# Kernel tuning notes

Measured on AMD Instinct MI355X. Metric: run time of the kernel, lower is better.

## Reference

```python
import jax, jax.numpy as jnp
import numpy as np
import math

H, HK, D = 16, 4, 128  # n_heads, n_kv_heads, head_dim
WINDOW = 1024
ROPE_BASE = 10000.0
EPS = 1e-6

def _rope_cos_sin(T, dtype):
    inv_freq = 1.0 / (ROPE_BASE ** (jnp.arange(0, D, 2, dtype=jnp.float32) / D))
    ang = jnp.arange(T, dtype=jnp.float32)[:, None] * inv_freq[None, :]  # [T, D/2]
    cos = jnp.concatenate([jnp.cos(ang), jnp.cos(ang)], axis=-1)  # [T, D]
    sin = jnp.concatenate([jnp.sin(ang), jnp.sin(ang)], axis=-1)
    return cos.astype(dtype), sin.astype(dtype)

def _rotate_half(x):
    x1, x2 = jnp.split(x, 2, axis=-1)
    return jnp.concatenate([-x2, x1], axis=-1)

def _apply_rope(t, cos, sin):
    # t: [B, h, T, D]; cos/sin: [T, D]
    return t * cos[None, None] + _rotate_half(t) * sin[None, None]

def setup_inputs() -> dict:
    key = jax.random.key(0)
    ks = jax.random.split(key, 7)
    d = H * D
    s = 1.0 / math.sqrt(d)
    return {
        "x": jax.random.normal(ks[0], (2, 2048, d), jnp.float32),
        "wq": jax.random.normal(ks[1], (H * D, d), jnp.float32) * s,
        "wk": jax.random.normal(ks[2], (HK * D, d), jnp.float32) * s,
        "wv": jax.random.normal(ks[3], (HK * D, d), jnp.float32) * s,
        "wo": jax.random.normal(ks[4], (d, H * D), jnp.float32) * s,
        "gamma_q": jnp.ones((D,), jnp.float32),
        "gamma_k": jnp.ones((D,), jnp.float32),
    }

def reference(x, wq, wk, wv, wo, gamma_q, gamma_k):
    B, T, d = x.shape
    G = H // HK  # query heads per kv head
    # projections (Linear stores [out, in]) -> [B, h, T, D]
    q = jnp.einsum('btd,ed->bte', x, wq).reshape(B, T, H, D).transpose(0, 2, 1, 3)
    k = jnp.einsum('btd,ed->bte', x, wk).reshape(B, T, HK, D).transpose(0, 2, 1, 3)
    v = jnp.einsum('btd,ed->bte', x, wv).reshape(B, T, HK, D).transpose(0, 2, 1, 3)
    cos, sin = _rope_cos_sin(T, x.dtype)
    q = _apply_rope(q, cos, sin)
    k = _apply_rope(k, cos, sin)
    # QK-norm: L2 normalize then learned per-dim scale
    q = q / (jnp.linalg.norm(q, axis=-1, keepdims=True) + EPS) * gamma_q
    k = k / (jnp.linalg.norm(k, axis=-1, keepdims=True) + EPS) * gamma_k
    # GQA: group query heads instead of materializing repeated K/V
    qg = q.reshape(B, HK, G, T, D)
    att = jnp.einsum('bkgtd,bksd->bkgts', qg, k) / math.sqrt(D)  # [B,HK,G,T,T]
    i = jnp.arange(T)
    diff = i[:, None] - i[None, :]
    bad = (diff < 0) | (diff > WINDOW)  # causal OR beyond sliding window
    att = jnp.where(bad[None, None, None], -jnp.inf, att)
    p = jax.nn.softmax(att, axis=-1)
    y = jnp.einsum('bkgts,bksd->bkgtd', p, v)  # [B,HK,G,T,D]
    y = y.reshape(B, H, T, D).transpose(0, 2, 1, 3).reshape(B, T, H * D)
    y = jnp.einsum('bte,de->btd', y, wo)
    return y
```

## Files before the change

kernel.cpp:

```cpp
#include <hip/hip_runtime.h>
#include <cstdint>
#include <cstddef>

typedef unsigned short u16;
typedef short bf16x8 __attribute__((ext_vector_type(8)));
typedef float f32x4 __attribute__((ext_vector_type(4)));

#define MFMA(a,b,c) __builtin_amdgcn_mfma_f32_16x16x32_bf16(a,b,c,0,0,0)

__device__ __forceinline__ u16 f2bf(float f) {
  unsigned u = __builtin_bit_cast(unsigned, f);
  u += 0x7fffu + ((u >> 16) & 1u);
  return (u16)(u >> 16);
}
__device__ __forceinline__ float bf2f(u16 b) {
  return __builtin_bit_cast(float, (unsigned)b << 16);
}
__device__ __forceinline__ float exp2_hw(float x) {
  float r;
  asm("v_exp_f32 %0, %1" : "=v"(r) : "v"(x));
  return r;
}
__device__ __forceinline__ void gl_lds16(const void* g, void* l) {
  __builtin_amdgcn_global_load_lds(
      (const __attribute__((address_space(1))) void*)g,
      (__attribute__((address_space(3))) void*)l, 16, 0, 0);
}
template <int N>
__device__ __forceinline__ void wait_vmcnt() {
  if constexpr (N == 0) asm volatile("s_waitcnt vmcnt(0)" ::: "memory");
  else if constexpr (N == 3) asm volatile("s_waitcnt vmcnt(3)" ::: "memory");
  else if constexpr (N == 4) asm volatile("s_waitcnt vmcnt(4)" ::: "memory");
}

__global__ __launch_bounds__(256) void cvt_all(const float* __restrict__ x,
                                               const float* __restrict__ wq,
                                               const float* __restrict__ wk,
                                               const float* __restrict__ wv,
                                               const float* __restrict__ wo,
                                               u16* __restrict__ xb,
                                               u16* __restrict__ wqkvb,
                                               u16* __restrict__ wob) {
  int idx = (blockIdx.x * 256 + threadIdx.x) * 4;
  const float* src;
  u16* dst;
  if (idx < 8388608) { src = x + idx; dst = xb + idx; }
  else if (idx < 12582912) { src = wq + (idx - 8388608); dst = wqkvb + (idx - 8388608); }
  else if (idx < 13631488) { src = wk + (idx - 12582912); dst = wqkvb + (idx - 8388608); }
  else if (idx < 14680064) { src = wv + (idx - 13631488); dst = wqkvb + (idx - 8388608); }
  else if (idx < 18874368) { src = wo + (idx - 14680064); dst = wob + (idx - 14680064); }
  else return;
  float4 v = *(const float4*)src;
  ushort4 o = {f2bf(v.x), f2bf(v.y), f2bf(v.z), f2bf(v.w)};
  *(ushort4*)dst = o;
}

__global__ __launch_bounds__(256) void rope_table(float* __restrict__ ctab,
                                                  float* __restrict__ stab) {
  int i = blockIdx.x * 256 + threadIdx.x;
  int t = i >> 6, f = i & 63;
  float inv_freq = powf(10000.0f, -(2.0f * f) / 128.0f);
  float ang = (float)t * inv_freq;
  ctab[i] = cosf(ang);
  stab[i] = sinf(ang);
}

template <int BM, int BN, int OUT_F32>
__global__ __launch_bounds__(512, 2) void gemm_nt8(const u16* __restrict__ A,
                                                   const u16* __restrict__ Bw,
                                                   void* __restrict__ Cout,
                                                   int M, int N, int K) {
  constexpr int PHASES = (BM * BN == 65536) ? 2 : 1;
  constexpr int WN = BN / 64;
  constexpr int WM = 8 / WN;
  constexpr int M_SUB = BM / WM;
  constexpr int M_REP = M_SUB / 16;
  constexpr int MRP = M_REP / PHASES;
  constexpr int ACH = BM / 128;
  constexpr int BCH = BN / 128;
  constexpr int LPT = ACH + BCH;

  __shared__ u16 As[3][BM * 32];
  __shared__ u16 Bs[3][BN * 32];

  const int tid = threadIdx.x;
  const int lane = tid & 63;
  const int wv = tid >> 6;
  const int l16 = lane & 15, lhi = lane >> 4;
  const int wm = wv / WN, wn = wv % WN;
  const int m0 = blockIdx.y * BM;
  const int n0 = blockIdx.x * BN;
  const int nt = K >> 5;

  const int srow = lane >> 2;
  const int scolb = ((lane & 3) * 16) ^ ((((lane >> 3) & 3)) << 4);

  auto stageA = [&](int buf, int kt, int ch) {
    const char* src = (const char*)A +
        ((size_t)(m0 + ch * 16 + srow) * K + (size_t)kt * 32) * 2 + scolb;
    gl_lds16(src, (char*)As[buf] + ch * 1024);
  };
  auto stageB = [&](int buf, int kt, int ch) {
    const char* src = (const char*)Bw +
        ((size_t)(n0 + ch * 16 + srow) * K + (size_t)kt * 32) * 2 + scolb;
    gl_lds16(src, (char*)Bs[buf] + ch * 1024);
  };
  auto readA = [&](const u16* Ab, int mi) -> bf16x8 {
    int row = wm * M_SUB + mi * 16 + l16;
    return *(const bf16x8*)((const char*)Ab + row * 64 +
                            ((lhi * 16) ^ (((row >> 1) & 3) << 4)));
  };
  auto readB = [&](const u16* Bb, int ni) -> bf16x8 {
    int row = wn * 64 + ni * 16 + l16;
    return *(const bf16x8*)((const char*)Bb + row * 64 +
                            ((lhi * 16) ^ (((row >> 1) & 3) << 4)));
  };

  f32x4 acc[M_REP][4] = {};

#pragma unroll
  for (int i = 0; i < ACH; ++i) stageA(0, 0, wv + 8 * i);
#pragma unroll
  for (int i = 0; i < BCH; ++i) stageB(0, 0, wv + 8 * i);
#pragma unroll
  for (int i = 0; i < ACH; ++i) stageA(1, 1, wv + 8 * i);
#pragma unroll
  for (int i = 0; i < BCH; ++i) stageB(1, 1, wv + 8 * i);
  wait_vmcnt<LPT>();
  __builtin_amdgcn_sched_barrier(0);
  __builtin_amdgcn_s_barrier();
  __builtin_amdgcn_sched_barrier(0);

  int p = 0;
  for (int t = 0; t < nt; ++t) {
    const u16* Ab = As[p];
    const u16* Bb = Bs[p];
    int pb = p + 2; if (pb >= 3) pb -= 3;
    const bool do_stage = (t + 2 < nt);

    bf16x8 bfrag[4], afrag[MRP];
#pragma unroll
    for (int ni = 0; ni < 4; ++ni) bfrag[ni] = readB(Bb, ni);
#pragma unroll
    for (int mi = 0; mi < MRP; ++mi) afrag[mi] = readA(Ab, mi);
    if (do_stage) {
#pragma unroll
      for (int i = 0; i < ACH; i += PHASES) stageA(pb, t + 2, wv + 8 * i);
#pragma unroll
      for (int i = 0; i < BCH; i += PHASES) stageB(pb, t + 2, wv + 8 * i);
    }
    if (PHASES == 1) { if (do_stage) wait_vmcnt<LPT>(); else wait_vmcnt<0>(); }
    __builtin_amdgcn_sched_barrier(0);
    __builtin_amdgcn_s_barrier();
    __builtin_amdgcn_sched_barrier(0);
    __builtin_amdgcn_s_setprio(1);
#pragma unroll
    for (int mi = 0; mi < MRP; ++mi)
#pragma unroll
      for (int ni = 0; ni < 4; ++ni)
        acc[mi][ni] = MFMA(afrag[mi], bfrag[ni], acc[mi][ni]);
    __builtin_amdgcn_s_setprio(0);
    __builtin_amdgcn_sched_barrier(0);
    __builtin_amdgcn_s_barrier();
    __builtin_amdgcn_sched_barrier(0);

    if (PHASES == 2) {
#pragma unroll
      for (int mi = 0; mi < MRP; ++mi) afrag[mi] = readA(Ab, MRP + mi);
      if (do_stage) {
#pragma unroll
        for (int i = 1; i < ACH; i += PHASES) stageA(pb, t + 2, wv + 8 * i);
#pragma unroll
        for (int i = 1; i < BCH; i += PHASES) stageB(pb, t + 2, wv + 8 * i);
      }
      if (do_stage) wait_vmcnt<LPT>(); else wait_vmcnt<0>();
      __builtin_amdgcn_sched_barrier(0);
      __builtin_amdgcn_s_barrier();
      __builtin_amdgcn_sched_barrier(0);
      __builtin_amdgcn_s_setprio(1);
#pragma unroll
      for (int mi = 0; mi < MRP; ++mi)
#pragma unroll
        for (int ni = 0; ni < 4; ++ni)
          acc[MRP + mi][ni] = MFMA(afrag[mi], bfrag[ni], acc[MRP + mi][ni]);
      __builtin_amdgcn_s_setprio(0);
      __builtin_amdgcn_sched_barrier(0);
      __builtin_amdgcn_s_barrier();
      __builtin_amdgcn_sched_barrier(0);
    }
    p = (p + 1 == 3) ? 0 : p + 1;
  }

#pragma unroll
  for (int mi = 0; mi < M_REP; ++mi)
#pragma unroll
    for (int ni = 0; ni < 4; ++ni) {
      int col = n0 + wn * 64 + ni * 16 + l16;
#pragma unroll
      for (int j = 0; j < 4; ++j) {
        int row = m0 + wm * M_SUB + mi * 16 + lhi * 4 + j;
        float v = acc[mi][ni][j];
        if (OUT_F32)
          ((float*)Cout)[(size_t)row * N + col] = v;
        else
          ((u16*)Cout)[(size_t)row * N + col] = f2bf(v);
      }
    }
}

template <int NH>
__global__ __launch_bounds__(256) void rope_norm(const u16* __restrict__ raw,
                                                 u16* __restrict__ out,
                                                 const float* __restrict__ ctab,
                                                 const float* __restrict__ stab,
                                                 const float* __restrict__ gamma,
                                                 int stride, int coloff, float scale) {
  int gw = blockIdx.x * 4 + (threadIdx.x >> 6);
  int lane = threadIdx.x & 63;
  int h = gw & (NH - 1);
  int bt = gw / NH;
  int t = bt & 2047, b = bt >> 11;
  const u16* r = raw + (size_t)bt * stride + coloff + (size_t)h * 128;
  float q1 = bf2f(r[lane]), q2 = bf2f(r[lane + 64]);
  float c = ctab[t * 64 + lane], s = stab[t * 64 + lane];
  float e1 = q1 * c - q2 * s;
  float e2 = q2 * c + q1 * s;
  float ss = e1 * e1 + e2 * e2;
#pragma unroll
  for (int off = 1; off < 64; off <<= 1) ss += __shfl_xor(ss, off);
  float inv = scale / (sqrtf(ss) + 1e-6f);
  size_t ob = (((size_t)(b * NH + h)) * 2048 + t) * 128;
  out[ob + lane]      = f2bf(e1 * inv * gamma[lane]);
  out[ob + lane + 64] = f2bf(e2 * inv * gamma[lane + 64]);
}

__global__ __launch_bounds__(256) void transpose_v(const u16* __restrict__ qkv,
                                                   u16* __restrict__ vt) {
  __shared__ u16 tile[32][33];
  int t0 = blockIdx.x * 32, d0 = blockIdx.y * 32;
  int bh = blockIdx.z;
  int b = bh >> 2, hkk = bh & 3;
  int tx = threadIdx.x & 31, ty = threadIdx.x >> 5;
#pragma unroll
  for (int i = 0; i < 4; ++i) {
    int r = ty + i * 8;
    tile[r][tx] = qkv[((size_t)(b * 2048 + t0 + r)) * 3072 + 2560 + hkk * 128 + d0 + tx];
  }
  __syncthreads();
#pragma unroll
  for (int i = 0; i < 4; ++i) {
    int r = ty + i * 8;
    vt[((size_t)((b * 4 + hkk) * 128 + d0 + r)) * 2048 + t0 + tx] = tile[tx][r];
  }
}

__global__ __launch_bounds__(512, 4) void attn_kernel(const u16* __restrict__ Qr,
                                                      const u16* __restrict__ Kr,
                                                      const u16* __restrict__ Vt,
                                                      u16* __restrict__ Yt) {
  __shared__ u16 Ks[2][64 * 128];
  __shared__ u16 Vs[2][128 * 64];
  __shared__ u16 Ps[8][16 * 64];
  const int tid = threadIdx.x;
  const int lane = tid & 63;
  const int wv = tid >> 6;
  const int l16 = lane & 15, lhi = lane >> 4;
  const int work = (blockIdx.x & 7) * 64 + (blockIdx.x >> 3);
  const int q0b = (work & 15) << 7;
  const int bh = work >> 4;
  const int b = bh >> 4, h = bh & 15;
  const int hk = h >> 2;
  const int q0w = q0b + wv * 16;

  const u16* qbase = Qr + (((size_t)bh) * 2048 + q0w + l16) * 128;
  bf16x8 qf[4];
#pragma unroll
  for (int dc = 0; dc < 4; ++dc)
    qf[dc] = *(const bf16x8*)(qbase + dc * 32 + lhi * 8);

  const char* kg = (const char*)(Kr + ((size_t)(b * 4 + hk)) * 2048 * 128);
  const u16* vg = Vt + ((size_t)(b * 4 + hk)) * 2048 * 128;

  auto stage = [&](int buf, int s0) {
#pragma unroll
    for (int i = 0; i < 2; ++i) {
      int c = wv + 8 * i;
      int row = c * 4 + lhi;
      int srcb = (l16 * 16) ^ ((row & 7) << 4);
      gl_lds16(kg + (size_t)(s0 + row) * 256 + srcb, (char*)Ks[buf] + c * 1024);
    }
    int r8 = lane >> 3, c8 = lane & 7;
#pragma unroll
    for (int i = 0; i < 2; ++i) {
      int c = wv + 8 * i;
      int row = c * 8 + r8;
      int srcb = (c8 * 16) ^ ((r8 & 7) << 4);
      gl_lds16((const char*)(vg + (size_t)row * 2048 + s0) + srcb,
               (char*)Vs[buf] + c * 1024);
    }
  };

  const bf16x8 ones = {0x3F80, 0x3F80, 0x3F80, 0x3F80, 0x3F80, 0x3F80, 0x3F80, 0x3F80};
  float mbase = 0.f;
  f32x4 lacc = {};
  f32x4 oacc[8] = {};

  int s_lo = q0b - 1024; if (s_lo < 0) s_lo = 0;
  const int nt = (q0b + 128 - s_lo) >> 6;

  stage(0, s_lo);
  __syncthreads();
  int cur = 0;
  for (int it = 0; it < nt; ++it) {
    const int s0 = s_lo + (it << 6);
    if (it + 1 < nt) stage(cur ^ 1, s0 + 64);
    const bool skip = (q0w + 15 < s0) || (q0w - (s0 + 63) > 1024);
    if (!skip) {
      f32x4 sacc[4] = {};
      const char* ksb = (const char*)Ks[cur];
      __builtin_amdgcn_s_setprio(1);
#pragma unroll
      for (int n = 0; n < 4; ++n) {
        int row = n * 16 + l16;
#pragma unroll
        for (int dc = 0; dc < 4; ++dc) {
          bf16x8 kf = *(const bf16x8*)(ksb + row * 256 +
                                       ((dc * 64 + lhi * 16) ^ ((l16 & 7) << 4)));
          sacc[n] = MFMA(qf[dc], kf, sacc[n]);
        }
      }
      __builtin_amdgcn_s_setprio(0);
      const bool domask = (q0w < s0 + 63) || (q0w + 15 - s0 > 1024);
      if (domask) {
#pragma unroll
        for (int n = 0; n < 4; ++n)
#pragma unroll
          for (int j = 0; j < 4; ++j) {
            int q = q0w + lhi * 4 + j;
            int s = s0 + n * 16 + l16;
            if ((unsigned)(q - s) > 1024u) sacc[n][j] = -INFINITY;
          }
      }
      float mt = sacc[0][0];
#pragma unroll
      for (int n = 0; n < 4; ++n)
#pragma unroll
        for (int j = 0; j < 4; ++j) mt = fmaxf(mt, sacc[n][j]);
#pragma unroll
      for (int off = 1; off < 64; off <<= 1) mt = fmaxf(mt, __shfl_xor(mt, off));
      if (mt > mbase + 8.f) {
        float sc2 = exp2_hw(mbase - mt);
#pragma unroll
        for (int j = 0; j < 4; ++j) lacc[j] *= sc2;
#pragma unroll
        for (int dt = 0; dt < 8; ++dt)
#pragma unroll
          for (int j = 0; j < 4; ++j) oacc[dt][j] *= sc2;
        mbase = mt;
      }
      char* psb = (char*)Ps[wv];
#pragma unroll
      for (int n = 0; n < 4; ++n)
#pragma unroll
        for (int j = 0; j < 4; ++j) {
          float p = exp2_hw(sacc[n][j] - mbase);
          int R = lhi * 4 + j;
          *(u16*)(psb + R * 128 + (((n * 16 + l16) * 2) ^ ((R & 7) << 4))) = f2bf(p);
        }
      bf16x8 pf[2];
#pragma unroll
      for (int kk = 0; kk < 2; ++kk)
        pf[kk] = *(const bf16x8*)(psb + l16 * 128 +
                                  ((kk * 64 + lhi * 16) ^ ((l16 & 7) << 4)));
      const char* vsb = (const char*)Vs[cur];
      __builtin_amdgcn_s_setprio(1);
      lacc = MFMA(pf[0], ones, lacc);
      lacc = MFMA(pf[1], ones, lacc);
#pragma unroll
      for (int dt = 0; dt < 8; ++dt) {
        int row = dt * 16 + l16;
#pragma unroll
        for (int kk = 0; kk < 2; ++kk) {
          bf16x8 vf = *(const bf16x8*)(vsb + row * 128 +
                                       ((kk * 64 + lhi * 16) ^ ((l16 & 7) << 4)));
          oacc[dt] = MFMA(pf[kk], vf, oacc[dt]);
        }
      }
      __builtin_amdgcn_s_setprio(0);
    }
    __syncthreads();
    cur ^= 1;
  }
#pragma unroll
  for (int j = 0; j < 4; ++j) {
    float inv = 1.0f / lacc[j];
    int q = q0w + lhi * 4 + j;
    size_t rowbase = ((size_t)(b * 2048 + q)) * 2048 + (size_t)h * 128;
#pragma unroll
    for (int dt = 0; dt < 8; ++dt)
      Yt[rowbase + dt * 16 + l16] = f2bf(oacc[dt][j] * inv);
  }
}

extern "C" void kernel_launch(void* const* d_in, const int* in_sizes, int n_in,
                              void* d_out, int out_size, void* d_ws, size_t ws_size,
                              hipStream_t stream) {
  (void)in_sizes; (void)n_in; (void)out_size; (void)ws_size;
  const float* x  = (const float*)d_in[0];
  const float* wq = (const float*)d_in[1];
  const float* wk = (const float*)d_in[2];
  const float* wv = (const float*)d_in[3];
  const float* wo = (const float*)d_in[4];
  const float* gq = (const float*)d_in[5];
  const float* gk = (const float*)d_in[6];
  float* out = (float*)d_out;
  char* ws = (char*)d_ws;

  size_t off = 0;
  auto alloc = [&](size_t bytes) {
    size_t o = off;
    off += (bytes + 255) & ~(size_t)255;
    return o;
  };
  u16* xb     = (u16*)(ws + alloc((size_t)4096 * 2048 * 2));
  u16* wqkvb  = (u16*)(ws + alloc((size_t)3072 * 2048 * 2));
  u16* wob    = (u16*)(ws + alloc((size_t)2048 * 2048 * 2));
  u16* qkvraw = (u16*)(ws + alloc((size_t)4096 * 3072 * 2));
  u16* qr     = (u16*)(ws + alloc((size_t)4096 * 2048 * 2));
  u16* kr     = (u16*)(ws + alloc((size_t)4096 * 512 * 2));
  u16* vt     = (u16*)(ws + alloc((size_t)4096 * 512 * 2));
  float* ctab = (float*)(ws + alloc((size_t)2048 * 64 * 4));
  float* stab = (float*)(ws + alloc((size_t)2048 * 64 * 4));
  u16* ytmp = qkvraw;

  const float sc_log2 = 0.12751744f;

  cvt_all<<<18432, 256, 0, stream>>>(x, wq, wk, wv, wo, xb, wqkvb, wob);
  rope_table<<<512, 256, 0, stream>>>(ctab, stab);

  gemm_nt8<256, 256, 0><<<dim3(12, 16), 512, 0, stream>>>(xb, wqkvb, qkvraw, 4096, 3072, 2048);

  rope_norm<16><<<16384, 256, 0, stream>>>(qkvraw, qr, ctab, stab, gq, 3072, 0, sc_log2);
  rope_norm<4><<<4096, 256, 0, stream>>>(qkvraw, kr, ctab, stab, gk, 3072, 2048, 1.0f);
  transpose_v<<<dim3(64, 4, 8), 256, 0, stream>>>(qkvraw, vt);

  attn_kernel<<<dim3(512), 512, 0, stream>>>(qr, kr, vt, ytmp);

  gemm_nt8<256, 128, 1><<<dim3(16, 16), 512, 0, stream>>>(ytmp, wob, out, 4096, 2048, 2048);
}
```

Baseline: 204.1 us.

## Software-pipeline GEMM LDS fragment reads with MFMA using double-buffered register fragments

Restructures both bf16 GEMM kernels' main loop so LDS reads for the next k-tile and global-to-LDS staging are interleaved with the two halves of MFMA work. B fragments are double-buffered in registers, and the loop is unrolled by two with a split A prefetch. Barriers drop from two or four per tile to two per tile with finer vmcnt waits. This aims to hide LDS read latency behind matrix ops, but raises register pressure and assumes nt is even.

```diff
diff --git a/kernel.cpp b/kernel.cpp
--- a/kernel.cpp
+++ b/kernel.cpp
@@ -29,6 +29,7 @@
 template <int N>
 __device__ __forceinline__ void wait_vmcnt() {
   if constexpr (N == 0) asm volatile("s_waitcnt vmcnt(0)" ::: "memory");
+  else if constexpr (N == 2) asm volatile("s_waitcnt vmcnt(2)" ::: "memory");
   else if constexpr (N == 3) asm volatile("s_waitcnt vmcnt(3)" ::: "memory");
   else if constexpr (N == 4) asm volatile("s_waitcnt vmcnt(4)" ::: "memory");
 }
@@ -66,19 +67,18 @@
 }
 
 template <int BM, int BN, int OUT_F32>
-__global__ __launch_bounds__(512, 2) void gemm_nt8(const u16* __restrict__ A,
-                                                   const u16* __restrict__ Bw,
-                                                   void* __restrict__ Cout,
-                                                   int M, int N, int K) {
-  constexpr int PHASES = (BM * BN == 65536) ? 2 : 1;
+__global__ __launch_bounds__(512, 2) void gemm8(const u16* __restrict__ A,
+                                                const u16* __restrict__ Bw,
+                                                void* __restrict__ Cout,
+                                                int M, int N, int K) {
   constexpr int WN = BN / 64;
   constexpr int WM = 8 / WN;
   constexpr int M_SUB = BM / WM;
-  constexpr int M_REP = M_SUB / 16;
-  constexpr int MRP = M_REP / PHASES;
-  constexpr int ACH = BM / 128;
-  constexpr int BCH = BN / 128;
-  constexpr int LPT = ACH + BCH;
+  constexpr int MF = M_SUB / 16;
+  constexpr int MH = MF / 2;
+  constexpr int ACH = BM / 16;
+  constexpr int TCH = (BM + BN) / 16 / 8;
+  constexpr int LPT = TCH;
 
   __shared__ u16 As[3][BM * 32];
   __shared__ u16 Bs[3][BN * 32];
@@ -95,15 +95,17 @@
   const int srow = lane >> 2;
   const int scolb = ((lane & 3) * 16) ^ ((((lane >> 3) & 3)) << 4);
 
-  auto stageA = [&](int buf, int kt, int ch) {
-    const char* src = (const char*)A +
-        ((size_t)(m0 + ch * 16 + srow) * K + (size_t)kt * 32) * 2 + scolb;
-    gl_lds16(src, (char*)As[buf] + ch * 1024);
-  };
-  auto stageB = [&](int buf, int kt, int ch) {
-    const char* src = (const char*)Bw +
-        ((size_t)(n0 + ch * 16 + srow) * K + (size_t)kt * 32) * 2 + scolb;
-    gl_lds16(src, (char*)Bs[buf] + ch * 1024);
+  auto stage_chunk = [&](int buf, int kt, int c) {
+    if (c < ACH) {
+      const char* src = (const char*)A +
+          ((size_t)(m0 + c * 16 + srow) * K + (size_t)kt * 32) * 2 + scolb;
+      gl_lds16(src, (char*)As[buf] + c * 1024);
+    } else {
+      int cc = c - ACH;
+      const char* src = (const char*)Bw +
+          ((size_t)(n0 + cc * 16 + srow) * K + (size_t)kt * 32) * 2 + scolb;
+      gl_lds16(src, (char*)Bs[buf] + cc * 1024);
+    }
   };
   auto readA = [&](const u16* Ab, int mi) -> bf16x8 {
     int row = wm * M_SUB + mi * 16 + l16;
@@ -116,83 +118,80 @@
                             ((lhi * 16) ^ (((row >> 1) & 3) << 4)));
   };
 
-  f32x4 acc[M_REP][4] = {};
-
-#pragma unroll
-  for (int i = 0; i < ACH; ++i) stageA(0, 0, wv + 8 * i);
-#pragma unroll
-  for (int i = 0; i < BCH; ++i) stageB(0, 0, wv + 8 * i);
-#pragma unroll
-  for (int i = 0; i < ACH; ++i) stageA(1, 1, wv + 8 * i);
-#pragma unroll
-  for (int i = 0; i < BCH; ++i) stageB(1, 1, wv + 8 * i);
+  f32x4 acc[MF][4] = {};
+  bf16x8 fB0[4], fB1[4], fA0[MH], fA1[MH];
+
+#pragma unroll
+  for (int i = 0; i < TCH; ++i) stage_chunk(0, 0, wv + 8 * i);
+#pragma unroll
+  for (int i = 0; i < TCH; ++i) stage_chunk(1, 1, wv + 8 * i);
   wait_vmcnt<LPT>();
   __builtin_amdgcn_sched_barrier(0);
   __builtin_amdgcn_s_barrier();
   __builtin_amdgcn_sched_barrier(0);
-
-  int p = 0;
-  for (int t = 0; t < nt; ++t) {
-    const u16* Ab = As[p];
-    const u16* Bb = Bs[p];
-    int pb = p + 2; if (pb >= 3) pb -= 3;
-    const bool do_stage = (t + 2 < nt);
-
-    bf16x8 bfrag[4], afrag[MRP];
-#pragma unroll
-    for (int ni = 0; ni < 4; ++ni) bfrag[ni] = readB(Bb, ni);
-#pragma unroll
-    for (int mi = 0; mi < MRP; ++mi) afrag[mi] = readA(Ab, mi);
-    if (do_stage) {
-#pragma unroll
-      for (int i = 0; i < ACH; i += PHASES) stageA(pb, t + 2, wv + 8 * i);
-#pragma unroll
-      for (int i = 0; i < BCH; i += PHASES) stageB(pb, t + 2, wv + 8 * i);
-    }
-    if (PHASES == 1) { if (do_stage) wait_vmcnt<LPT>(); else wait_vmcnt<0>(); }
+#pragma unroll
+  for (int ni = 0; ni < 4; ++ni) fB0[ni] = readB(Bs[0], ni);
+#pragma unroll
+  for (int mi = 0; mi < MH; ++mi) fA0[mi] = readA(As[0], mi);
+#pragma unroll
+  for (int mi = 0; mi < MH; ++mi) fA1[mi] = readA(As[0], MH + mi);
+
+  auto tile_body = [&](int t, int p, bf16x8* Bc, bf16x8* Bn) {
+    int pn = p + 1; if (pn == 3) pn = 0;
+    int ps = pn + 1; if (ps == 3) ps = 0;
+    const bool rd = (t + 1 < nt);
+    const bool st = (t + 2 < nt);
+    __builtin_amdgcn_s_setprio(1);
+#pragma unroll
+    for (int mi = 0; mi < MH; ++mi)
+#pragma unroll
+      for (int ni = 0; ni < 4; ++ni)
+        acc[mi][ni] = MFMA(fA0[mi], Bc[ni], acc[mi][ni]);
+    __builtin_amdgcn_s_setprio(0);
+    if (st) {
+      stage_chunk(ps, t + 2, wv);
+      stage_chunk(ps, t + 2, wv + 8);
+    }
+    if (rd) {
+      if (st) wait_vmcnt<2>(); else wait_vmcnt<0>();
+      __builtin_amdgcn_sched_barrier(0);
+      __builtin_amdgcn_s_barrier();
+      __builtin_amdgcn_sched_barrier(0);
+#pragma unroll
+      for (int ni = 0; ni < 4; ++ni) Bn[ni] = readB(Bs[pn], ni);
+#pragma unroll
+      for (int mi = 0; mi < MH; ++mi) fA0[mi] = readA(As[pn], mi);
+    }
+    __builtin_amdgcn_s_setprio(1);
+#pragma unroll
+    for (int mi = 0; mi < MH; ++mi)
+#pragma unroll
+      for (int ni = 0; ni < 4; ++ni)
+        acc[MH + mi][ni] = MFMA(fA1[mi], Bc[ni], acc[MH + mi][ni]);
+    __builtin_amdgcn_s_setprio(0);
+    if (st) {
+#pragma unroll
+      for (int i = 2; i < TCH; ++i) stage_chunk(ps, t + 2, wv + 8 * i);
+    }
     __builtin_amdgcn_sched_barrier(0);
     __builtin_amdgcn_s_barrier();
     __builtin_amdgcn_sched_barrier(0);
-    __builtin_amdgcn_s_setprio(1);
-#pragma unroll
-    for (int mi = 0; mi < MRP; ++mi)
-#pragma unroll
-      for (int ni = 0; ni < 4; ++ni)
-        acc[mi][ni] = MFMA(afrag[mi], bfrag[ni], acc[mi][ni]);
-    __builtin_amdgcn_s_setprio(0);
-    __builtin_amdgcn_sched_barrier(0);
-    __builtin_amdgcn_s_barrier();
-    __builtin_amdgcn_sched_barrier(0);
-
-    if (PHASES == 2) {
-#pragma unroll
-      for (int mi = 0; mi < MRP; ++mi) afrag[mi] = readA(Ab, MRP + mi);
-      if (do_stage) {
-#pragma unroll
-        for (int i = 1; i < ACH; i += PHASES) stageA(pb, t + 2, wv + 8 * i);
-#pragma unroll
-        for (int i = 1; i < BCH; i += PHASES) stageB(pb, t + 2, wv + 8 * i);
-      }
-      if (do_stage) wait_vmcnt<LPT>(); else wait_vmcnt<0>();
-      __builtin_amdgcn_sched_barrier(0);
-      __builtin_amdgcn_s_barrier();
-      __builtin_amdgcn_sched_barrier(0);
-      __builtin_amdgcn_s_setprio(1);
-#pragma unroll
-      for (int mi = 0; mi < MRP; ++mi)
-#pragma unroll
-        for (int ni = 0; ni < 4; ++ni)
-          acc[MRP + mi][ni] = MFMA(afrag[mi], bfrag[ni], acc[MRP + mi][ni]);
-      __builtin_amdgcn_s_setprio(0);
-      __builtin_amdgcn_sched_barrier(0);
-      __builtin_amdgcn_s_barrier();
-      __builtin_amdgcn_sched_barrier(0);
-    }
-    p = (p + 1 == 3) ? 0 : p + 1;
+    if (rd) {
+#pragma unroll
+      for (int mi = 0; mi < MH; ++mi) fA1[mi] = readA(As[pn], MH + mi);
+    }
+  };
+
+  int pc = 0;
+  for (int t = 0; t < nt; t += 2) {
+    tile_body(t, pc, fB0, fB1);
+    int p1 = pc + 1; if (p1 == 3) p1 = 0;
+    tile_body(t + 1, p1, fB1, fB0);
+    pc = p1 + 1; if (pc == 3) pc = 0;
   }
 
 #pragma unroll
-  for (int mi = 0; mi < M_REP; ++mi)
+  for (int mi = 0; mi < MF; ++mi)
 #pragma unroll
     for (int ni = 0; ni < 4; ++ni) {
       int col = n0 + wn * 64 + ni * 16 + l16;
@@ -438,7 +437,7 @@
   cvt_all<<<18432, 256, 0, stream>>>(x, wq, wk, wv, wo, xb, wqkvb, wob);
   rope_table<<<512, 256, 0, stream>>>(ctab, stab);
 
-  gemm_nt8<256, 256, 0><<<dim3(12, 16), 512, 0, stream>>>(xb, wqkvb, qkvraw, 4096, 3072, 2048);
+  gemm8<256, 256, 0><<<dim3(12, 16), 512, 0, stream>>>(xb, wqkvb, qkvraw, 4096, 3072, 2048);
 
   rope_norm<16><<<16384, 256, 0, stream>>>(qkvraw, qr, ctab, stab, gq, 3072, 0, sc_log2);
   rope_norm<4><<<4096, 256, 0, stream>>>(qkvraw, kr, ctab, stab, gk, 3072, 2048, 1.0f);
@@ -446,5 +445,5 @@
 
   attn_kernel<<<dim3(512), 512, 0, stream>>>(qr, kr, vt, ytmp);
 
-  gemm_nt8<256, 128, 1><<<dim3(16, 16), 512, 0, stream>>>(ytmp, wob, out, 4096, 2048, 2048);
-}
+  gemm8<256, 128, 1><<<dim3(16, 16), 512, 0, stream>>>(ytmp, wob, out, 4096, 2048, 2048);
+}
```

New measurement: 223.1 us. +9.3%, slower.

## Replace GEMM with 256x256 BK=64 double-buffered kernel and vectorize rope_norm

Applied to the files above, without the earlier changes.

The old three-buffer BK=32 GEMM template is replaced by a single 256x256 tile kernel that stages BK=64 slices into double-buffered LDS. Each K-step is split into two MFMA halves, with global-to-LDS staging issued between them. The output projection now also uses 256x256 tiles, which halves its grid to 128 blocks and may underfill the device. rope_norm is also rewritten to load packed bf16 pairs and exchange rotate-half partners through a lane shuffle, giving vectorized reads and writes.

```diff
diff --git a/kernel.cpp b/kernel.cpp
--- a/kernel.cpp
+++ b/kernel.cpp
@@ -29,8 +29,7 @@
 template <int N>
 __device__ __forceinline__ void wait_vmcnt() {
   if constexpr (N == 0) asm volatile("s_waitcnt vmcnt(0)" ::: "memory");
-  else if constexpr (N == 3) asm volatile("s_waitcnt vmcnt(3)" ::: "memory");
-  else if constexpr (N == 4) asm volatile("s_waitcnt vmcnt(4)" ::: "memory");
+  else if constexpr (N == 8) asm volatile("s_waitcnt vmcnt(8)" ::: "memory");
 }
 
 __global__ __launch_bounds__(256) void cvt_all(const float* __restrict__ x,
@@ -65,140 +64,111 @@
   stab[i] = sinf(ang);
 }
 
-template <int BM, int BN, int OUT_F32>
-__global__ __launch_bounds__(512, 2) void gemm_nt8(const u16* __restrict__ A,
-                                                   const u16* __restrict__ Bw,
-                                                   void* __restrict__ Cout,
-                                                   int M, int N, int K) {
-  constexpr int PHASES = (BM * BN == 65536) ? 2 : 1;
-  constexpr int WN = BN / 64;
-  constexpr int WM = 8 / WN;
-  constexpr int M_SUB = BM / WM;
-  constexpr int M_REP = M_SUB / 16;
-  constexpr int MRP = M_REP / PHASES;
-  constexpr int ACH = BM / 128;
-  constexpr int BCH = BN / 128;
-  constexpr int LPT = ACH + BCH;
-
-  __shared__ u16 As[3][BM * 32];
-  __shared__ u16 Bs[3][BN * 32];
-
+template <int OUT_F32>
+__global__ __launch_bounds__(512, 2) void gemm8p(const u16* __restrict__ A,
+                                                 const u16* __restrict__ Bw,
+                                                 void* __restrict__ Cout,
+                                                 int M, int N, int K) {
+  __shared__ u16 As[2][2][128 * 64];
+  __shared__ u16 Bs[2][2][128 * 64];
   const int tid = threadIdx.x;
   const int lane = tid & 63;
   const int wv = tid >> 6;
   const int l16 = lane & 15, lhi = lane >> 4;
-  const int wm = wv / WN, wn = wv % WN;
-  const int m0 = blockIdx.y * BM;
-  const int n0 = blockIdx.x * BN;
-  const int nt = K >> 5;
-
-  const int srow = lane >> 2;
-  const int scolb = ((lane & 3) * 16) ^ ((((lane >> 3) & 3)) << 4);
-
-  auto stageA = [&](int buf, int kt, int ch) {
-    const char* src = (const char*)A +
-        ((size_t)(m0 + ch * 16 + srow) * K + (size_t)kt * 32) * 2 + scolb;
-    gl_lds16(src, (char*)As[buf] + ch * 1024);
+  const int wm = wv >> 2, wn = wv & 3;
+  const int m0 = blockIdx.y * 256;
+  const int n0 = blockIdx.x * 256;
+  const int nt = K >> 6;
+
+  const int srow8 = lane >> 3;
+  const int scol = ((lane & 7) * 16) ^ (srow8 << 4);
+
+  auto stage_tile = [&](int buf, int kt) {
+#pragma unroll
+    for (int h = 0; h < 2; ++h)
+#pragma unroll
+      for (int s = 0; s < 2; ++s) {
+        int ch = wv + 8 * s;
+        int row = m0 + h * 128 + ch * 8 + srow8;
+        const char* src = (const char*)A + ((size_t)row * K + (size_t)kt * 64) * 2 + scol;
+        gl_lds16(src, (char*)As[buf][h] + ch * 1024);
+      }
+#pragma unroll
+    for (int h = 0; h < 2; ++h)
+#pragma unroll
+      for (int s = 0; s < 2; ++s) {
+        int ch = wv + 8 * s;
+        int row = n0 + h * 128 + ch * 8 + srow8;
+        const char* src = (const char*)Bw + ((size_t)row * K + (size_t)kt * 64) * 2 + scol;
+        gl_lds16(src, (char*)Bs[buf][h] + ch * 1024);
+      }
   };
-  auto stageB = [&](int buf, int kt, int ch) {
-    const char* src = (const char*)Bw +
-        ((size_t)(n0 + ch * 16 + srow) * K + (size_t)kt * 32) * 2 + scolb;
-    gl_lds16(src, (char*)Bs[buf] + ch * 1024);
+  auto readA = [&](int buf, int mi, int kk) -> bf16x8 {
+    int lr = mi * 16 + l16;
+    return *(const bf16x8*)((const char*)As[buf][wm] + lr * 128 +
+                            ((kk * 64 + lhi * 16) ^ ((l16 & 7) << 4)));
   };
-  auto readA = [&](const u16* Ab, int mi) -> bf16x8 {
-    int row = wm * M_SUB + mi * 16 + l16;
-    return *(const bf16x8*)((const char*)Ab + row * 64 +
-                            ((lhi * 16) ^ (((row >> 1) & 3) << 4)));
+  auto readB = [&](int buf, int ni, int kk) -> bf16x8 {
+    int lr = (wn & 1) * 64 + ni * 16 + l16;
+    return *(const bf16x8*)((const char*)Bs[buf][wn >> 1] + lr * 128 +
+                            ((kk * 64 + lhi * 16) ^ ((l16 & 7) << 4)));
   };
-  auto readB = [&](const u16* Bb, int ni) -> bf16x8 {
-    int row = wn * 64 + ni * 16 + l16;
-    return *(const bf16x8*)((const char*)Bb + row * 64 +
-                            ((lhi * 16) ^ (((row >> 1) & 3) << 4)));
-  };
-
-  f32x4 acc[M_REP][4] = {};
-
-#pragma unroll
-  for (int i = 0; i < ACH; ++i) stageA(0, 0, wv + 8 * i);
-#pragma unroll
-  for (int i = 0; i < BCH; ++i) stageB(0, 0, wv + 8 * i);
-#pragma unroll
-  for (int i = 0; i < ACH; ++i) stageA(1, 1, wv + 8 * i);
-#pragma unroll
-  for (int i = 0; i < BCH; ++i) stageB(1, 1, wv + 8 * i);
-  wait_vmcnt<LPT>();
+
+  f32x4 acc[8][4] = {};
+
+  stage_tile(0, 0);
+  stage_tile(1, 1);
+  wait_vmcnt<8>();
   __builtin_amdgcn_sched_barrier(0);
   __builtin_amdgcn_s_barrier();
   __builtin_amdgcn_sched_barrier(0);
 
-  int p = 0;
   for (int t = 0; t < nt; ++t) {
-    const u16* Ab = As[p];
-    const u16* Bb = Bs[p];
-    int pb = p + 2; if (pb >= 3) pb -= 3;
-    const bool do_stage = (t + 2 < nt);
-
-    bf16x8 bfrag[4], afrag[MRP];
-#pragma unroll
-    for (int ni = 0; ni < 4; ++ni) bfrag[ni] = readB(Bb, ni);
-#pragma unroll
-    for (int mi = 0; mi < MRP; ++mi) afrag[mi] = readA(Ab, mi);
-    if (do_stage) {
-#pragma unroll
-      for (int i = 0; i < ACH; i += PHASES) stageA(pb, t + 2, wv + 8 * i);
-#pragma unroll
-      for (int i = 0; i < BCH; i += PHASES) stageB(pb, t + 2, wv + 8 * i);
-    }
-    if (PHASES == 1) { if (do_stage) wait_vmcnt<LPT>(); else wait_vmcnt<0>(); }
+    const int b = t & 1;
+    bf16x8 bf0[4], af0[8];
+#pragma unroll
+    for (int ni = 0; ni < 4; ++ni) bf0[ni] = readB(b, ni, 0);
+#pragma unroll
+    for (int mi = 0; mi < 8; ++mi) af0[mi] = readA(b, mi, 0);
+    __builtin_amdgcn_s_setprio(1);
+#pragma unroll
+    for (int mi = 0; mi < 8; ++mi)
+#pragma unroll
+      for (int ni = 0; ni < 4; ++ni)
+        acc[mi][ni] = MFMA(af0[mi], bf0[ni], acc[mi][ni]);
+    __builtin_amdgcn_s_setprio(0);
+    bf16x8 bf1[4], af1[8];
+#pragma unroll
+    for (int ni = 0; ni < 4; ++ni) bf1[ni] = readB(b, ni, 1);
+#pragma unroll
+    for (int mi = 0; mi < 8; ++mi) af1[mi] = readA(b, mi, 1);
+    asm volatile("s_waitcnt lgkmcnt(0)" ::: "memory");
     __builtin_amdgcn_sched_barrier(0);
     __builtin_amdgcn_s_barrier();
     __builtin_amdgcn_sched_barrier(0);
+    if (t + 2 < nt) stage_tile(b, t + 2);
     __builtin_amdgcn_s_setprio(1);
 #pragma unroll
-    for (int mi = 0; mi < MRP; ++mi)
+    for (int mi = 0; mi < 8; ++mi)
 #pragma unroll
       for (int ni = 0; ni < 4; ++ni)
-        acc[mi][ni] = MFMA(afrag[mi], bfrag[ni], acc[mi][ni]);
+        acc[mi][ni] = MFMA(af1[mi], bf1[ni], acc[mi][ni]);
     __builtin_amdgcn_s_setprio(0);
+    if (t + 2 < nt) wait_vmcnt<8>();
+    else if (t + 1 < nt) wait_vmcnt<0>();
     __builtin_amdgcn_sched_barrier(0);
     __builtin_amdgcn_s_barrier();
     __builtin_amdgcn_sched_barrier(0);
-
-    if (PHASES == 2) {
-#pragma unroll
-      for (int mi = 0; mi < MRP; ++mi) afrag[mi] = readA(Ab, MRP + mi);
-      if (do_stage) {
-#pragma unroll
-        for (int i = 1; i < ACH; i += PHASES) stageA(pb, t + 2, wv + 8 * i);
-#pragma unroll
-        for (int i = 1; i < BCH; i += PHASES) stageB(pb, t + 2, wv + 8 * i);
-      }
-      if (do_stage) wait_vmcnt<LPT>(); else wait_vmcnt<0>();
-      __builtin_amdgcn_sched_barrier(0);
-      __builtin_amdgcn_s_barrier();
-      __builtin_amdgcn_sched_barrier(0);
-      __builtin_amdgcn_s_setprio(1);
-#pragma unroll
-      for (int mi = 0; mi < MRP; ++mi)
-#pragma unroll
-        for (int ni = 0; ni < 4; ++ni)
-          acc[MRP + mi][ni] = MFMA(afrag[mi], bfrag[ni], acc[MRP + mi][ni]);
-      __builtin_amdgcn_s_setprio(0);
-      __builtin_amdgcn_sched_barrier(0);
-      __builtin_amdgcn_s_barrier();
-      __builtin_amdgcn_sched_barrier(0);
-    }
-    p = (p + 1 == 3) ? 0 : p + 1;
   }
 
 #pragma unroll
-  for (int mi = 0; mi < M_REP; ++mi)
+  for (int mi = 0; mi < 8; ++mi)
 #pragma unroll
     for (int ni = 0; ni < 4; ++ni) {
       int col = n0 + wn * 64 + ni * 16 + l16;
 #pragma unroll
       for (int j = 0; j < 4; ++j) {
-        int row = m0 + wm * M_SUB + mi * 16 + lhi * 4 + j;
+        int row = m0 + wm * 128 + mi * 16 + lhi * 4 + j;
         float v = acc[mi][ni][j];
         if (OUT_F32)
           ((float*)Cout)[(size_t)row * N + col] = v;
@@ -219,19 +189,27 @@
   int lane = threadIdx.x & 63;
   int h = gw & (NH - 1);
   int bt = gw / NH;
-  int t = bt & 2047, b = bt >> 11;
+  int t = bt & 2047, bb = bt >> 11;
   const u16* r = raw + (size_t)bt * stride + coloff + (size_t)h * 128;
-  float q1 = bf2f(r[lane]), q2 = bf2f(r[lane + 64]);
-  float c = ctab[t * 64 + lane], s = stab[t * 64 + lane];
-  float e1 = q1 * c - q2 * s;
-  float e2 = q2 * c + q1 * s;
-  float ss = e1 * e1 + e2 * e2;
+  ushort2 own = *(const ushort2*)(r + 2 * lane);
+  int pk = __shfl_xor(__builtin_bit_cast(int, own), 32);
+  ushort2 par = __builtin_bit_cast(ushort2, pk);
+  float x0 = bf2f(own.x), x1 = bf2f(own.y);
+  float y0 = bf2f(par.x), y1 = bf2f(par.y);
+  int f = (lane & 31) * 2;
+  float2 c2 = *(const float2*)(ctab + t * 64 + f);
+  float2 s2 = *(const float2*)(stab + t * 64 + f);
+  bool hi = lane >= 32;
+  float e0 = hi ? (x0 * c2.x + y0 * s2.x) : (x0 * c2.x - y0 * s2.x);
+  float e1 = hi ? (x1 * c2.y + y1 * s2.y) : (x1 * c2.y - y1 * s2.y);
+  float ss = e0 * e0 + e1 * e1;
 #pragma unroll
   for (int off = 1; off < 64; off <<= 1) ss += __shfl_xor(ss, off);
   float inv = scale / (sqrtf(ss) + 1e-6f);
-  size_t ob = (((size_t)(b * NH + h)) * 2048 + t) * 128;
-  out[ob + lane]      = f2bf(e1 * inv * gamma[lane]);
-  out[ob + lane + 64] = f2bf(e2 * inv * gamma[lane + 64]);
+  float2 g2 = *(const float2*)(gamma + 2 * lane);
+  size_t ob = (((size_t)(bb * NH + h)) * 2048 + t) * 128 + 2 * lane;
+  ushort2 o = {f2bf(e0 * inv * g2.x), f2bf(e1 * inv * g2.y)};
+  *(ushort2*)(out + ob) = o;
 }
 
 __global__ __launch_bounds__(256) void transpose_v(const u16* __restrict__ qkv,
@@ -438,7 +416,7 @@
   cvt_all<<<18432, 256, 0, stream>>>(x, wq, wk, wv, wo, xb, wqkvb, wob);
   rope_table<<<512, 256, 0, stream>>>(ctab, stab);
 
-  gemm_nt8<256, 256, 0><<<dim3(12, 16), 512, 0, stream>>>(xb, wqkvb, qkvraw, 4096, 3072, 2048);
+  gemm8p<0><<<dim3(12, 16), 512, 0, stream>>>(xb, wqkvb, qkvraw, 4096, 3072, 2048);
 
   rope_norm<16><<<16384, 256, 0, stream>>>(qkvraw, qr, ctab, stab, gq, 3072, 0, sc_log2);
   rope_norm<4><<<4096, 256, 0, stream>>>(qkvraw, kr, ctab, stab, gk, 3072, 2048, 1.0f);
@@ -446,5 +424,5 @@
 
   attn_kernel<<<dim3(512), 512, 0, stream>>>(qr, kr, vt, ytmp);
 
-  gemm_nt8<256, 128, 1><<<dim3(16, 16), 512, 0, stream>>>(ytmp, wob, out, 4096, 2048, 2048);
-}
+  gemm8p<1><<<dim3(8, 16), 512, 0, stream>>>(ytmp, wob, out, 4096, 2048, 2048);
+}
```

New measurement: 211.6 us. 3.7% more time.
